# Performance work log

Measured on AMD Instinct MI355X. Metric: run time of the kernel, lower is better.

Reference implementation:

```python
import jax, jax.numpy as jnp
import numpy as np

B, T, D, V, SPK = 8, 4096, 512, 1024, 512
DECAY = 0.95
COARSE_SCALE = 0.2
RES_SCALE = 0.35
MAX_LS = 1.2
MAX_SIL = 0.35
COLD_RUNS = 2.0
MIN_DUR = 2.0


def gelu(x):
    return jax.nn.gelu(x, approximate=False)


def setup_inputs() -> dict:
    key = jax.random.key(0)
    ks = jax.random.split(key, 24)
    def n(k, shape, s=1.0):
        return jax.random.normal(k, shape, dtype=jnp.float32) * s
    inp = {}
    inp['content_units'] = jax.random.randint(ks[0], (B, T), 0, V)
    inp['log_anchor'] = n(ks[1], (B, T), 0.5) + 1.0
    inp['unit_mask'] = jax.random.randint(ks[2], (B, T), 0, 2)
    inp['sealed_mask'] = jax.random.randint(ks[3], (B, T), 0, 2)
    inp['silence_mask'] = jax.random.randint(ks[4], (B, T), 0, 2)
    inp['sep_hint'] = jax.random.uniform(ks[5], (B, T), dtype=jnp.float32)
    inp['edge_cue'] = jax.random.uniform(ks[6], (B, T), dtype=jnp.float32)
    inp['run_stability'] = jax.random.uniform(ks[7], (B, T), dtype=jnp.float32)
    inp['global_rate'] = n(ks[8], (B,), 0.1) + 1.0
    inp['local_rate_ema'] = n(ks[9], (B, 1), 0.1) + 1.0
    inp['spk_embed'] = n(ks[10], (B, SPK))
    s = 0.02
    inp['emb_table'] = n(ks[11], (V, D), s)
    inp['feat_W'] = n(ks[12], (5, D), s)      # scalar features -> dim
    inp['feat_b'] = jnp.zeros((D,), jnp.float32)
    inp['spk_W'] = n(ks[13], (SPK, D), s)
    inp['spk_b'] = jnp.zeros((D,), jnp.float32)
    inp['coarse_W1'] = n(ks[14], (D + 1, D), s)
    inp['coarse_b1'] = jnp.zeros((D,), jnp.float32)
    inp['coarse_W2'] = n(ks[15], (D, 1), s)
    inp['coarse_b2'] = jnp.zeros((1,), jnp.float32)
    inp['res_W1'] = n(ks[16], (2 * D + 1, D), s)
    inp['res_b1'] = jnp.zeros((D,), jnp.float32)
    inp['res_W2'] = n(ks[17], (D, 1), s)
    inp['res_b2'] = jnp.zeros((1,), jnp.float32)
    inp['src_rate_init'] = jnp.zeros((1,), jnp.float32)
    return inp


def _local_rate_scan(observed_log, speech_mask, init_rate):
    # Causal masked exponential-decay recurrence: emitted rate at t is the
    # state BEFORE observing step t (strictly causal); state only updates on
    # speech-commit steps.
    def step(rate, xs):
        obs, m = xs  # [B], [B]
        new = jnp.where(m > 0, DECAY * rate + (1.0 - DECAY) * obs, rate)
        return new, rate
    final, seq = jax.lax.scan(step, init_rate, (observed_log.T, speech_mask.T))
    return seq.T, final[:, None]  # [B,T], [B,1]


def reference(content_units, log_anchor, unit_mask, sealed_mask, silence_mask,
              sep_hint, edge_cue, run_stability, global_rate, local_rate_ema,
              spk_embed, emb_table, feat_W, feat_b, spk_W, spk_b,
              coarse_W1, coarse_b1, coarse_W2, coarse_b2,
              res_W1, res_b1, res_W2, res_b2, src_rate_init):
    f32 = jnp.float32
    mask = jnp.clip(unit_mask.astype(f32), 0.0, 1.0)
    sealed = jnp.clip(sealed_mask.astype(f32), 0.0, 1.0)
    silence = jnp.clip(silence_mask.astype(f32), 0.0, 1.0) * mask
    stability = jnp.clip(run_stability.astype(f32), 0.0, 1.0) * mask
    commit = mask * sealed
    sil_commit = commit * silence
    speech = commit * (1.0 - silence)

    la = log_anchor.astype(f32)
    rate_seq, rate_final = _local_rate_scan(la, speech, local_rate_ema[:, 0].astype(f32))

    # CausalUnitRunEncoder: token embedding + projection of per-step scalars
    feats = jnp.stack([la, rate_seq, silence, sep_hint.astype(f32), edge_cue.astype(f32)], axis=-1)  # [B,T,5]
    query = gelu(emb_table[content_units] + feats @ feat_W + feat_b) * mask[..., None]  # [B,T,D]

    grc = global_rate.astype(f32).reshape(-1, 1)[:, :1]  # [B,1]
    spk_ctx = jnp.tanh(spk_embed.astype(f32) @ spk_W + spk_b)  # [B,D]

    gsa = (grc - rate_seq) * commit  # global_shift_analytic [B,T]
    coarse_in = jnp.concatenate([spk_ctx, grc], axis=-1)  # [B,D+1]
    coarse_scalar = COARSE_SCALE * jnp.tanh((gelu(coarse_in @ coarse_W1 + coarse_b1) @ coarse_W2 + coarse_b2)[:, 0])  # [B]
    coarse_corr = coarse_scalar[:, None] * commit
    global_term = (gsa + coarse_corr) * commit

    # residual head: split first-layer weights to avoid materializing the concat
    Wq, Ws, wg = res_W1[:D], res_W1[D:2 * D], res_W1[2 * D]
    h = gelu(query @ Wq + (spk_ctx @ Ws)[:, None, :] + global_term[..., None] * wg + res_b1)  # [B,T,D]
    residual = RES_SCALE * jnp.tanh((h @ res_W2 + res_b2)[..., 0])  # [B,T]

    prefix_prev = jnp.maximum(jnp.cumsum(speech, axis=1) - speech, 0.0)
    cold_gate = jnp.clip(prefix_prev / COLD_RUNS, 0.0, 1.0)
    short_gate = jnp.clip((jnp.maximum(jnp.exp(la), 1.0) - 1.0) / max(1.0, MIN_DUR - 1.0), 0.0, 1.0)
    residual_gate = cold_gate * short_gate * stability * speech
    residual = residual * residual_gate

    pred_speech = jnp.clip(global_term + residual, -MAX_LS, MAX_LS) * speech
    pred_silence = jnp.clip(global_term, -MAX_SIL, MAX_SIL) * sil_commit
    pred = pred_speech + pred_silence  # unit_logstretch [B,T]
    return pred
```

## Files before the change

### kernel.cpp

```cpp
#include <hip/hip_runtime.h>
#include <hip/hip_bf16.h>

#define BB 8
#define TT 4096
#define DD 512
#define MM (BB*TT)
#define DECAYF 0.95f
#define OMDECAYF (1.0f - 0.95f)

typedef __attribute__((ext_vector_type(8))) short bf16x8;
typedef __attribute__((ext_vector_type(4))) float f32x4;

__device__ __forceinline__ float gelu_f(float x){
  return 0.5f * x * (1.0f + erff(x * 0.70710678118654752f));
}

__device__ __forceinline__ unsigned f2bf(float x){
  unsigned u = __float_as_uint(x);
  return (u + 0x7FFFu + ((u >> 16) & 1u)) >> 16;
}

__global__ __launch_bounds__(512) void pre_kernel(
    const float* __restrict__ spk_embed, const float* __restrict__ spk_W,
    const float* __restrict__ spk_b, const float* __restrict__ rW1,
    const float* __restrict__ la_g, const int* __restrict__ um,
    const int* __restrict__ sm, const int* __restrict__ zm,
    const float* __restrict__ stab_g, const float* __restrict__ lre,
    float* __restrict__ spk_ctx, unsigned short* __restrict__ wqt,
    float* __restrict__ rate_seq, float* __restrict__ rgate_a,
    int* __restrict__ active_list, int* __restrict__ acount)
{
  __shared__ float se[DD];
  __shared__ float red[8][64];
  __shared__ float tile[64][65];
  __shared__ float wAg[8], wBg[8], wSg[8];
  __shared__ int wcnt[8];
  int blk = blockIdx.x, t = threadIdx.x;
  int lane = t & 63, wid = t >> 6;

  if (blk < 64){
    int b = blk >> 3, d0 = (blk & 7) * 64;
    int dl = lane, ks = wid;
    se[t] = spk_embed[b*DD + t];
    __syncthreads();
    float a = 0.f;
    const float* wp = spk_W + (long)(ks*64)*DD + d0 + dl;
    #pragma unroll 8
    for (int k = 0; k < 64; ++k) a += se[ks*64 + k] * wp[(long)k*DD];
    red[ks][dl] = a;
    __syncthreads();
    if (t < 64){
      float s = spk_b[d0 + t];
      #pragma unroll
      for (int i = 0; i < 8; ++i) s += red[i][t];
      spk_ctx[b*DD + d0 + t] = tanhf(s);
    }
    return;
  }
  if (blk < 128){
    int tb = blk - 64;
    int nb = (tb & 7) * 64, kb = (tb >> 3) * 64;
    int tx = t & 63, ty = t >> 6;
    #pragma unroll
    for (int i = 0; i < 8; ++i){
      int k = ty + i*8;
      tile[k][tx] = rW1[(long)(kb + k)*DD + nb + tx];
    }
    __syncthreads();
    #pragma unroll
    for (int i = 0; i < 8; ++i){
      int nl = ty + i*8;
      wqt[(long)(nb + nl)*DD + kb + tx] = (unsigned short)f2bf(tile[tx][nl]);
    }
    return;
  }

  int b = blk - 128;
  int base = b*TT + t*8;
  float4 la0 = *(const float4*)(la_g + base);
  float4 la1 = *(const float4*)(la_g + base + 4);
  int4 u0 = *(const int4*)(um + base), u1 = *(const int4*)(um + base + 4);
  int4 s0 = *(const int4*)(sm + base), s1 = *(const int4*)(sm + base + 4);
  int4 z0 = *(const int4*)(zm + base), z1 = *(const int4*)(zm + base + 4);
  float4 st0 = *(const float4*)(stab_g + base), st1 = *(const float4*)(stab_g + base + 4);
  float lav[8] = {la0.x,la0.y,la0.z,la0.w,la1.x,la1.y,la1.z,la1.w};
  int uv[8] = {u0.x,u0.y,u0.z,u0.w,u1.x,u1.y,u1.z,u1.w};
  int sv[8] = {s0.x,s0.y,s0.z,s0.w,s1.x,s1.y,s1.z,s1.w};
  int zv[8] = {z0.x,z0.y,z0.z,z0.w,z1.x,z1.y,z1.z,z1.w};
  float stv_[8] = {st0.x,st0.y,st0.z,st0.w,st1.x,st1.y,st1.z,st1.w};
  float spv[8], stv[8];

  float A = 1.f, Bv = 0.f, S = 0.f;
  #pragma unroll
  for (int i = 0; i < 8; ++i){
    float m = uv[i] > 0 ? 1.f : 0.f;
    float sealed = sv[i] > 0 ? 1.f : 0.f;
    float sil = (zv[i] > 0 ? 1.f : 0.f) * m;
    float speech = (m * sealed) * (1.f - sil);
    spv[i] = speech;
    stv[i] = fminf(fmaxf(stv_[i], 0.f), 1.f) * m;
    if (speech > 0.f){
      Bv = DECAYF*Bv + OMDECAYF*lav[i];
      A *= DECAYF;
      S += 1.f;
    }
  }
  #pragma unroll
  for (int d = 1; d < 64; d <<= 1){
    float Au = __shfl_up(A, d, 64);
    float Bu = __shfl_up(Bv, d, 64);
    float Su = __shfl_up(S, d, 64);
    if (lane >= d){ Bv = A*Bu + Bv; A = A*Au; S += Su; }
  }
  if (lane == 63){ wAg[wid] = A; wBg[wid] = Bv; wSg[wid] = S; }
  float Ale = __shfl_up(A, 1, 64), Ble = __shfl_up(Bv, 1, 64), Sle = __shfl_up(S, 1, 64);
  if (lane == 0){ Ale = 1.f; Ble = 0.f; Sle = 0.f; }
  __syncthreads();
  float Awp = 1.f, Bwp = 0.f, Swp = 0.f;
  for (int w = 0; w < wid; ++w){
    Bwp = wAg[w]*Bwp + wBg[w];
    Awp = wAg[w]*Awp;
    Swp += wSg[w];
  }
  float Bex = Ale*Bwp + Ble;
  float Aex = Ale*Awp;
  float Sex = Swp + Sle;

  float rate = Aex*lre[b] + Bex;
  float ps = Sex;
  float ro[8], rg[8];
  #pragma unroll
  for (int i = 0; i < 8; ++i){
    ro[i] = rate;
    float cold = fminf(ps * 0.5f, 1.f);
    float shortg = fminf(fmaxf(expf(lav[i]) - 1.f, 0.f), 1.f);
    rg[i] = cold * shortg * stv[i] * spv[i];
    if (spv[i] > 0.f){
      rate = DECAYF*rate + OMDECAYF*lav[i];
      ps += 1.f;
    }
  }
  *(float4*)(rate_seq + base)     = make_float4(ro[0],ro[1],ro[2],ro[3]);
  *(float4*)(rate_seq + base + 4) = make_float4(ro[4],ro[5],ro[6],ro[7]);
  *(float4*)(rgate_a + base)      = make_float4(rg[0],rg[1],rg[2],rg[3]);
  *(float4*)(rgate_a + base + 4)  = make_float4(rg[4],rg[5],rg[6],rg[7]);

  int nact = 0;
  #pragma unroll
  for (int i = 0; i < 8; ++i) nact += (rg[i] != 0.f) ? 1 : 0;
  int inc = nact;
  #pragma unroll
  for (int d = 1; d < 64; d <<= 1){
    int u = __shfl_up(inc, d, 64);
    if (lane >= d) inc += u;
  }
  int myex = inc - nact;
  if (lane == 63) wcnt[wid] = inc;
  __syncthreads();
  int wbase = 0;
  for (int w = 0; w < wid; ++w) wbase += wcnt[w];
  int pos = wbase + myex;
  int* alist = active_list + b*TT;
  #pragma unroll
  for (int i = 0; i < 8; ++i){
    if (rg[i] != 0.f) alist[pos++] = base + i;
  }
  if (t == 0){
    int total = 0;
    #pragma unroll
    for (int w = 0; w < 8; ++w) total += wcnt[w];
    acount[b] = total;
  }
}

__global__ __launch_bounds__(512) void mid_kernel(
    const float* __restrict__ spk_ctx, const float* __restrict__ rW1,
    const float* __restrict__ cW1, const float* __restrict__ cb1,
    const float* __restrict__ cW2, const float* __restrict__ grate,
    const int* __restrict__ content, const float* __restrict__ la_g,
    const float* __restrict__ sep, const float* __restrict__ edge,
    const float* __restrict__ emb, const float* __restrict__ fW,
    const float* __restrict__ fb, const float* __restrict__ rate_seq,
    const int* __restrict__ active_list, const int* __restrict__ acount,
    float* __restrict__ s_vec, float* __restrict__ coarse_part,
    unsigned short* __restrict__ wsQ)
{
  int blk = blockIdx.x, t = threadIdx.x;
  int lane = t & 63, wid = t >> 6;

  if (blk < 64){
    __shared__ float sc[DD];
    __shared__ float red1[8][64];
    __shared__ float red2[8][64];
    int b = blk >> 3, d0 = (blk & 7) * 64;
    int dl = lane, ks = wid;
    sc[t] = spk_ctx[b*DD + t];
    __syncthreads();
    float a1 = 0.f, a2 = 0.f;
    const float* wsp = rW1 + (long)(DD + ks*64)*DD + d0 + dl;
    const float* wcp = cW1 + (long)(ks*64)*DD + d0 + dl;
    #pragma unroll 4
    for (int k = 0; k < 64; ++k){
      float s = sc[ks*64 + k];
      a1 += s * wsp[(long)k*DD];
      a2 += s * wcp[(long)k*DD];
    }
    red1[ks][dl] = a1; red2[ks][dl] = a2;
    __syncthreads();
    if (t < 64){
      int d = d0 + t;
      float s1 = 0.f;
      float s2 = cb1[d] + grate[b] * cW1[(long)DD*DD + d];
      #pragma unroll
      for (int i = 0; i < 8; ++i){ s1 += red1[i][t]; s2 += red2[i][t]; }
      s_vec[b*DD + d] = s1;
      float hv = gelu_f(s2) * cW2[d];
      #pragma unroll
      for (int sh = 1; sh < 64; sh <<= 1) hv += __shfl_xor(hv, sh, 64);
      if (t == 0) coarse_part[blk] = hv;
    }
    return;
  }

  int tb = blk - 64;
  int b = tb >> 6;
  int slot0 = (tb & 63) * 8 + wid;
  int cnt = acount[b];
  const int* alist = active_list + b*TT;
  int c0 = lane * 8;
  for (int j = slot0; j < cnt; j += 512){
    int gr = alist[j];
    float la = la_g[gr], rate = rate_seq[gr];
    float sepv = sep[gr], edgev = edge[gr];
    const float* er = emb + (long)content[gr]*DD + c0;
    float4 e0 = *(const float4*)(er), e1 = *(const float4*)(er + 4);
    float4 w00 = *(const float4*)(fW + c0),        w01 = *(const float4*)(fW + c0 + 4);
    float4 w10 = *(const float4*)(fW + DD + c0),   w11 = *(const float4*)(fW + DD + c0 + 4);
    float4 w30 = *(const float4*)(fW + 3*DD + c0), w31 = *(const float4*)(fW + 3*DD + c0 + 4);
    float4 w40 = *(const float4*)(fW + 4*DD + c0), w41 = *(const float4*)(fW + 4*DD + c0 + 4);
    float4 b0 = *(const float4*)(fb + c0), b1 = *(const float4*)(fb + c0 + 4);
    unsigned v0 = f2bf(gelu_f(e0.x + la*w00.x + rate*w10.x + sepv*w30.x + edgev*w40.x + b0.x));
    unsigned v1 = f2bf(gelu_f(e0.y + la*w00.y + rate*w10.y + sepv*w30.y + edgev*w40.y + b0.y));
    unsigned v2 = f2bf(gelu_f(e0.z + la*w00.z + rate*w10.z + sepv*w30.z + edgev*w40.z + b0.z));
    unsigned v3 = f2bf(gelu_f(e0.w + la*w00.w + rate*w10.w + sepv*w30.w + edgev*w40.w + b0.w));
    unsigned v4 = f2bf(gelu_f(e1.x + la*w01.x + rate*w11.x + sepv*w31.x + edgev*w41.x + b1.x));
    unsigned v5 = f2bf(gelu_f(e1.y + la*w01.y + rate*w11.y + sepv*w31.y + edgev*w41.y + b1.y));
    unsigned v6 = f2bf(gelu_f(e1.z + la*w01.z + rate*w11.z + sepv*w31.z + edgev*w41.z + b1.z));
    unsigned v7 = f2bf(gelu_f(e1.w + la*w01.w + rate*w11.w + sepv*w31.w + edgev*w41.w + b1.w));
    int4 pkv = make_int4((int)((v1 << 16) | v0), (int)((v3 << 16) | v2),
                         (int)((v5 << 16) | v4), (int)((v7 << 16) | v6));
    *(int4*)(wsQ + (long)(b*TT + j)*DD + c0) = pkv;
  }
}

__global__ __launch_bounds__(512) void main_kernel(
    const float* __restrict__ rate_seq, const unsigned short* __restrict__ wsQ,
    const unsigned short* __restrict__ wqt,
    const float* __restrict__ s_vec, const float* __restrict__ rW1,
    const float* __restrict__ rb1, const float* __restrict__ rW2,
    const float* __restrict__ rb2, const float* __restrict__ grate,
    const float* __restrict__ coarse_part, const float* __restrict__ cb2,
    const int* __restrict__ um, const int* __restrict__ sm,
    const int* __restrict__ zm,
    const float* __restrict__ rgate_a, const int* __restrict__ active_list,
    const int* __restrict__ acount, float* __restrict__ out)
{
  __shared__ unsigned short Af[16*32*32];
  __shared__ unsigned short Bs[2][512*32];
  __shared__ float part[8][32];
  __shared__ int seg_sh[3];
  int blk = blockIdx.x, tid = threadIdx.x, wid = tid >> 6, lane = tid & 63;

  if (tid < 128){
    int gr = blk*128 + tid;
    float rgv = rgate_a[gr];
    if (rgv == 0.f){
      int b = gr >> 12;
      float csum = cb2[0];
      #pragma unroll
      for (int c = 0; c < 8; ++c) csum += coarse_part[b*8 + c];
      float cs = 0.2f * tanhf(csum);
      float m = um[gr] > 0 ? 1.f : 0.f;
      float sealed = sm[gr] > 0 ? 1.f : 0.f;
      float sil = (zm[gr] > 0 ? 1.f : 0.f) * m;
      float commit = m * sealed;
      float speech = commit * (1.f - sil);
      float silc = commit * sil;
      float g = (grate[b] - rate_seq[gr] + cs) * commit;
      out[gr] = fminf(fmaxf(g, -1.2f), 1.2f) * speech
              + fminf(fmaxf(g, -0.35f), 0.35f) * silc;
    }
  }

  const char* wbase = (const char*)wqt;
  auto stageB = [&](unsigned short* dstbuf, int kc){
    int k0b = kc * 64;
    #pragma unroll
    for (int i = 0; i < 4; ++i){
      int j = wid*4 + i;
      int n = j*16 + (lane >> 2);
      int slot = (lane & 3) ^ ((n >> 1) & 3);
      const char* src = wbase + (long)n*1024 + k0b + slot*16;
      char* dst = (char*)dstbuf + j*1024 + (lane << 4);
      __builtin_amdgcn_global_load_lds(
          (const __attribute__((address_space(1))) void*)src,
          (__attribute__((address_space(3))) void*)dst, 16, 0, 0);
    }
  };

  for (int p = blk; ; p += 256){
    if (tid == 0){
      int cum = 0, sb = -1, slo = 0, scnt = 0;
      #pragma unroll
      for (int b = 0; b < BB; ++b){
        int c = acount[b];
        int nb = (c + 31) >> 5;
        if (sb < 0 && p < cum + nb){ sb = b; slo = (p - cum) * 32; scnt = c; }
        cum += nb;
      }
      seg_sh[0] = sb; seg_sh[1] = slo; seg_sh[2] = scnt;
    }
    __syncthreads();
    int seg_b = seg_sh[0], seg_lo = seg_sh[1], seg_cnt = seg_sh[2];
    if (seg_b < 0) break;
    const int* alist = active_list + seg_b*TT;
    const char* qseg = (const char*)(wsQ + (long)(seg_b*TT + seg_lo)*DD);

    float csum = cb2[0];
    #pragma unroll
    for (int c = 0; c < 8; ++c) csum += coarse_part[seg_b*8 + c];
    float cs = 0.2f * tanhf(csum);
    float grc = grate[seg_b];

    #pragma unroll
    for (int i = 0; i < 4; ++i){
      int idx = wid + i*8;
      int kcA = idx >> 1, half = idx & 1;
      int row = half*16 + (lane >> 2);
      int slot = (lane & 3) ^ ((row >> 1) & 3);
      const char* src = qseg + (long)row*1024 + kcA*64 + slot*16;
      char* dst = (char*)Af + kcA*2048 + half*1024 + (lane << 4);
      __builtin_amdgcn_global_load_lds(
          (const __attribute__((address_space(1))) void*)src,
          (__attribute__((address_space(3))) void*)dst, 16, 0, 0);
    }
    stageB(&Bs[0][0], 0);
    asm volatile("s_waitcnt vmcnt(0)" ::: "memory");
    __syncthreads();

    f32x4 acc[2][4];
    #pragma unroll
    for (int i = 0; i < 2; ++i)
      #pragma unroll
      for (int j = 0; j < 4; ++j) acc[i][j] = (f32x4){0.f,0.f,0.f,0.f};

    int rgp = lane >> 4, li = lane & 15;
    #pragma unroll
    for (int kc = 0; kc < 16; ++kc){
      if (kc < 15) stageB(&Bs[(kc+1)&1][0], kc+1);
      if (kc < 15) asm volatile("s_waitcnt vmcnt(4)" ::: "memory");
      else         asm volatile("s_waitcnt vmcnt(0)" ::: "memory");
      const char* bsb = (const char*)&Bs[kc&1][0];
      bf16x8 a[2], bb[4];
      #pragma unroll
      for (int mt = 0; mt < 2; ++mt){
        int row = mt*16 + li;
        int slot = rgp ^ ((row >> 1) & 3);
        a[mt] = *(const bf16x8*)((const char*)Af + kc*2048 + row*64 + (slot << 4));
      }
      #pragma unroll
      for (int nt = 0; nt < 4; ++nt){
        int n = wid*64 + nt*16 + li;
        int slot = rgp ^ ((n >> 1) & 3);
        bb[nt] = *(const bf16x8*)(bsb + n*64 + slot*16);
      }
      #pragma unroll
      for (int mt = 0; mt < 2; ++mt)
        #pragma unroll
        for (int nt = 0; nt < 4; ++nt)
          acc[mt][nt] = __builtin_amdgcn_mfma_f32_16x16x32_bf16(a[mt], bb[nt], acc[mt][nt], 0, 0, 0);
    }

    float svv[4], wgv[4], b1v[4], w2v[4];
    #pragma unroll
    for (int nt = 0; nt < 4; ++nt){
      int j = wid*64 + nt*16 + li;
      svv[nt] = s_vec[seg_b*DD + j];
      wgv[nt] = rW1[1024*DD + j];
      b1v[nt] = rb1[j];
      w2v[nt] = rW2[j];
    }
    #pragma unroll
    for (int mt = 0; mt < 2; ++mt){
      #pragma unroll
      for (int r = 0; r < 4; ++r){
        int row = mt*16 + rgp*4 + r;
        int q = seg_lo + row; if (q > seg_cnt-1) q = seg_cnt-1;
        int gr = alist[q];
        float gt = grc - rate_seq[gr] + cs;
        float s = 0.f;
        #pragma unroll
        for (int nt = 0; nt < 4; ++nt){
          float y = acc[mt][nt][r] + svv[nt] + gt*wgv[nt] + b1v[nt];
          s += gelu_f(y) * w2v[nt];
        }
        s += __shfl_xor(s, 1, 64);
        s += __shfl_xor(s, 2, 64);
        s += __shfl_xor(s, 4, 64);
        s += __shfl_xor(s, 8, 64);
        if (li == 0) part[wid][row] = s;
      }
    }
    __syncthreads();
    if (tid < 32){
      int q = seg_lo + tid;
      if (q < seg_cnt){
        int gr = alist[q];
        float s = 0.f;
        #pragma unroll
        for (int w = 0; w < 8; ++w) s += part[w][tid];
        float resid = 0.35f * tanhf(s + rb2[0]) * rgate_a[gr];
        float g = grc - rate_seq[gr] + cs;
        out[gr] = fminf(fmaxf(g + resid, -1.2f), 1.2f);
      }
    }
    __syncthreads();
  }
}

extern "C" void kernel_launch(void* const* d_in, const int* in_sizes, int n_in,
                              void* d_out, int out_size, void* d_ws, size_t ws_size,
                              hipStream_t stream)
{
  const int*   content = (const int*)  d_in[0];
  const float* la      = (const float*)d_in[1];
  const int*   um      = (const int*)  d_in[2];
  const int*   smk     = (const int*)  d_in[3];
  const int*   zm      = (const int*)  d_in[4];
  const float* sep     = (const float*)d_in[5];
  const float* edge    = (const float*)d_in[6];
  const float* stab    = (const float*)d_in[7];
  const float* grate   = (const float*)d_in[8];
  const float* lre     = (const float*)d_in[9];
  const float* spk_e   = (const float*)d_in[10];
  const float* emb     = (const float*)d_in[11];
  const float* fW      = (const float*)d_in[12];
  const float* fb      = (const float*)d_in[13];
  const float* spk_W   = (const float*)d_in[14];
  const float* spk_b   = (const float*)d_in[15];
  const float* cW1     = (const float*)d_in[16];
  const float* cb1     = (const float*)d_in[17];
  const float* cW2     = (const float*)d_in[18];
  const float* cb2     = (const float*)d_in[19];
  const float* rW1     = (const float*)d_in[20];
  const float* rb1     = (const float*)d_in[21];
  const float* rW2     = (const float*)d_in[22];
  const float* rb2     = (const float*)d_in[23];

  char* w = (char*)d_ws;
  unsigned short* wsQ   = (unsigned short*)(w);
  unsigned short* wsWqT = (unsigned short*)(w + 33554432);
  size_t off = 33554432 + 524288;
  float* rate_seq = (float*)(w + off); off += MM*4;
  float* rgate_a  = (float*)(w + off); off += MM*4;
  int*   active_list = (int*)(w + off); off += MM*4;
  float* s_vec    = (float*)(w + off); off += BB*DD*4;
  float* spk_ctx  = (float*)(w + off); off += BB*DD*4;
  float* coarse_part = (float*)(w + off); off += 64*4;
  int*   acount   = (int*)(w + off); off += 256;

  pre_kernel<<<136, 512, 0, stream>>>(spk_e, spk_W, spk_b, rW1,
      la, um, smk, zm, stab, lre,
      spk_ctx, wsWqT, rate_seq, rgate_a, active_list, acount);
  mid_kernel<<<576, 512, 0, stream>>>(spk_ctx, rW1, cW1, cb1, cW2, grate,
      content, la, sep, edge, emb, fW, fb, rate_seq, active_list, acount,
      s_vec, coarse_part, wsQ);
  main_kernel<<<256, 512, 0, stream>>>(rate_seq, wsQ, wsWqT,
      s_vec, rW1, rb1, rW2, rb2, grate, coarse_part, cb2,
      um, smk, zm, rgate_a, active_list, acount, (float*)d_out);
}
```

Measured before the change: 35.32 us.

## Pack per-token gating data into float4 and precompute segment map for main kernel

The pre kernel now writes one packed float4 per token: the global term without the coarse correction, the speech mask, the silence mask and the residual gate. The main kernel reads this instead of re-reading the three mask arrays, rate_seq, grate and rgate_a. An extra block in the mid kernel precomputes a segment-to-batch map, so the main kernel no longer needs a per-iteration thread-0 scan and barrier. The tail clamp on segment rows is dropped. A memset of the active list is added so padded rows read index 0, which is safe because token 0 always has a zero gate. The cost is an extra memset launch and a larger packed buffer in the workspace.

```diff
diff --git a/kernel.cpp b/kernel.cpp
--- a/kernel.cpp
+++ b/kernel.cpp
@@ -26,8 +26,9 @@
     const float* __restrict__ la_g, const int* __restrict__ um,
     const int* __restrict__ sm, const int* __restrict__ zm,
     const float* __restrict__ stab_g, const float* __restrict__ lre,
+    const float* __restrict__ grate,
     float* __restrict__ spk_ctx, unsigned short* __restrict__ wqt,
-    float* __restrict__ rate_seq, float* __restrict__ rgate_a,
+    float* __restrict__ rate_seq, float4* __restrict__ pk4,
     int* __restrict__ active_list, int* __restrict__ acount)
 {
   __shared__ float se[DD];
@@ -88,7 +89,7 @@
   int sv[8] = {s0.x,s0.y,s0.z,s0.w,s1.x,s1.y,s1.z,s1.w};
   int zv[8] = {z0.x,z0.y,z0.z,z0.w,z1.x,z1.y,z1.z,z1.w};
   float stv_[8] = {st0.x,st0.y,st0.z,st0.w,st1.x,st1.y,st1.z,st1.w};
-  float spv[8], stv[8];
+  float spv[8], slv[8], stv[8];
 
   float A = 1.f, Bv = 0.f, S = 0.f;
   #pragma unroll
@@ -96,8 +97,9 @@
     float m = uv[i] > 0 ? 1.f : 0.f;
     float sealed = sv[i] > 0 ? 1.f : 0.f;
     float sil = (zv[i] > 0 ? 1.f : 0.f) * m;
-    float speech = (m * sealed) * (1.f - sil);
-    spv[i] = speech;
+    float commit = m * sealed;
+    float speech = commit * (1.f - sil);
+    spv[i] = speech; slv[i] = commit * sil;
     stv[i] = fminf(fmaxf(stv_[i], 0.f), 1.f) * m;
     if (speech > 0.f){
       Bv = DECAYF*Bv + OMDECAYF*lav[i];
@@ -128,13 +130,17 @@
 
   float rate = Aex*lre[b] + Bex;
   float ps = Sex;
+  float grc = grate[b];
   float ro[8], rg[8];
   #pragma unroll
   for (int i = 0; i < 8; ++i){
     ro[i] = rate;
+    float commit = spv[i] + slv[i];
+    float gA = (grc - rate) * commit;
     float cold = fminf(ps * 0.5f, 1.f);
     float shortg = fminf(fmaxf(expf(lav[i]) - 1.f, 0.f), 1.f);
     rg[i] = cold * shortg * stv[i] * spv[i];
+    pk4[base + i] = make_float4(gA, spv[i], slv[i], rg[i]);
     if (spv[i] > 0.f){
       rate = DECAYF*rate + OMDECAYF*lav[i];
       ps += 1.f;
@@ -142,8 +148,6 @@
   }
   *(float4*)(rate_seq + base)     = make_float4(ro[0],ro[1],ro[2],ro[3]);
   *(float4*)(rate_seq + base + 4) = make_float4(ro[4],ro[5],ro[6],ro[7]);
-  *(float4*)(rgate_a + base)      = make_float4(rg[0],rg[1],rg[2],rg[3]);
-  *(float4*)(rgate_a + base + 4)  = make_float4(rg[4],rg[5],rg[6],rg[7]);
 
   int nact = 0;
   #pragma unroll
@@ -183,7 +187,7 @@
     const float* __restrict__ fb, const float* __restrict__ rate_seq,
     const int* __restrict__ active_list, const int* __restrict__ acount,
     float* __restrict__ s_vec, float* __restrict__ coarse_part,
-    unsigned short* __restrict__ wsQ)
+    unsigned short* __restrict__ wsQ, int2* __restrict__ segmap)
 {
   int blk = blockIdx.x, t = threadIdx.x;
   int lane = t & 63, wid = t >> 6;
@@ -218,6 +222,25 @@
       #pragma unroll
       for (int sh = 1; sh < 64; sh <<= 1) hv += __shfl_xor(hv, sh, 64);
       if (t == 0) coarse_part[blk] = hv;
+    }
+    return;
+  }
+  if (blk == 576){
+    int cnts[BB], offs[BB];
+    int cum = 0;
+    #pragma unroll
+    for (int b = 0; b < BB; ++b){
+      cnts[b] = (acount[b] + 31) >> 5;
+      offs[b] = cum;
+      cum += cnts[b];
+    }
+    for (int i = t; i < 1024; i += 512){
+      int2 e = make_int2(-1, 0);
+      #pragma unroll
+      for (int b = 0; b < BB; ++b){
+        if (i >= offs[b] && i < offs[b] + cnts[b]) e = make_int2(b, (i - offs[b]) * 32);
+      }
+      segmap[i] = e;
     }
     return;
   }
@@ -254,41 +277,32 @@
 }
 
 __global__ __launch_bounds__(512) void main_kernel(
-    const float* __restrict__ rate_seq, const unsigned short* __restrict__ wsQ,
-    const unsigned short* __restrict__ wqt,
+    const unsigned short* __restrict__ wsQ, const unsigned short* __restrict__ wqt,
     const float* __restrict__ s_vec, const float* __restrict__ rW1,
     const float* __restrict__ rb1, const float* __restrict__ rW2,
-    const float* __restrict__ rb2, const float* __restrict__ grate,
+    const float* __restrict__ rb2,
     const float* __restrict__ coarse_part, const float* __restrict__ cb2,
-    const int* __restrict__ um, const int* __restrict__ sm,
-    const int* __restrict__ zm,
-    const float* __restrict__ rgate_a, const int* __restrict__ active_list,
-    const int* __restrict__ acount, float* __restrict__ out)
+    const float4* __restrict__ pk4, const int* __restrict__ active_list,
+    const int2* __restrict__ segmap, float* __restrict__ out)
 {
   __shared__ unsigned short Af[16*32*32];
   __shared__ unsigned short Bs[2][512*32];
   __shared__ float part[8][32];
-  __shared__ int seg_sh[3];
   int blk = blockIdx.x, tid = threadIdx.x, wid = tid >> 6, lane = tid & 63;
 
   if (tid < 128){
     int gr = blk*128 + tid;
-    float rgv = rgate_a[gr];
-    if (rgv == 0.f){
+    float4 pk = pk4[gr];
+    if (pk.w == 0.f){
       int b = gr >> 12;
       float csum = cb2[0];
       #pragma unroll
       for (int c = 0; c < 8; ++c) csum += coarse_part[b*8 + c];
       float cs = 0.2f * tanhf(csum);
-      float m = um[gr] > 0 ? 1.f : 0.f;
-      float sealed = sm[gr] > 0 ? 1.f : 0.f;
-      float sil = (zm[gr] > 0 ? 1.f : 0.f) * m;
-      float commit = m * sealed;
-      float speech = commit * (1.f - sil);
-      float silc = commit * sil;
-      float g = (grate[b] - rate_seq[gr] + cs) * commit;
-      out[gr] = fminf(fmaxf(g, -1.2f), 1.2f) * speech
-              + fminf(fmaxf(g, -0.35f), 0.35f) * silc;
+      float commit = pk.y + pk.z;
+      float g = pk.x + cs * commit;
+      out[gr] = fminf(fmaxf(g, -1.2f), 1.2f) * pk.y
+              + fminf(fmaxf(g, -0.35f), 0.35f) * pk.z;
     }
   }
 
@@ -308,21 +322,10 @@
     }
   };
 
-  for (int p = blk; ; p += 256){
-    if (tid == 0){
-      int cum = 0, sb = -1, slo = 0, scnt = 0;
-      #pragma unroll
-      for (int b = 0; b < BB; ++b){
-        int c = acount[b];
-        int nb = (c + 31) >> 5;
-        if (sb < 0 && p < cum + nb){ sb = b; slo = (p - cum) * 32; scnt = c; }
-        cum += nb;
-      }
-      seg_sh[0] = sb; seg_sh[1] = slo; seg_sh[2] = scnt;
-    }
-    __syncthreads();
-    int seg_b = seg_sh[0], seg_lo = seg_sh[1], seg_cnt = seg_sh[2];
-    if (seg_b < 0) break;
+  for (int p = blk; p < 1024; p += 256){
+    int2 seg = segmap[p];
+    if (seg.x < 0) break;
+    int seg_b = seg.x, seg_lo = seg.y;
     const int* alist = active_list + seg_b*TT;
     const char* qseg = (const char*)(wsQ + (long)(seg_b*TT + seg_lo)*DD);
 
@@ -330,7 +333,6 @@
     #pragma unroll
     for (int c = 0; c < 8; ++c) csum += coarse_part[seg_b*8 + c];
     float cs = 0.2f * tanhf(csum);
-    float grc = grate[seg_b];
 
     #pragma unroll
     for (int i = 0; i < 4; ++i){
@@ -395,9 +397,9 @@
       #pragma unroll
       for (int r = 0; r < 4; ++r){
         int row = mt*16 + rgp*4 + r;
-        int q = seg_lo + row; if (q > seg_cnt-1) q = seg_cnt-1;
+        int q = seg_lo + row;
         int gr = alist[q];
-        float gt = grc - rate_seq[gr] + cs;
+        float gt = pk4[gr].x + cs;
         float s = 0.f;
         #pragma unroll
         for (int nt = 0; nt < 4; ++nt){
@@ -414,13 +416,14 @@
     __syncthreads();
     if (tid < 32){
       int q = seg_lo + tid;
-      if (q < seg_cnt){
-        int gr = alist[q];
+      int gr = alist[q];
+      float4 pk = pk4[gr];
+      if (pk.w != 0.f){
         float s = 0.f;
         #pragma unroll
         for (int w = 0; w < 8; ++w) s += part[w][tid];
-        float resid = 0.35f * tanhf(s + rb2[0]) * rgate_a[gr];
-        float g = grc - rate_seq[gr] + cs;
+        float resid = 0.35f * tanhf(s + rb2[0]) * pk.w;
+        float g = pk.x + cs;
         out[gr] = fminf(fmaxf(g + resid, -1.2f), 1.2f);
       }
     }
@@ -462,20 +465,22 @@
   unsigned short* wsWqT = (unsigned short*)(w + 33554432);
   size_t off = 33554432 + 524288;
   float* rate_seq = (float*)(w + off); off += MM*4;
-  float* rgate_a  = (float*)(w + off); off += MM*4;
+  float4* pk4     = (float4*)(w + off); off += MM*16;
   int*   active_list = (int*)(w + off); off += MM*4;
   float* s_vec    = (float*)(w + off); off += BB*DD*4;
   float* spk_ctx  = (float*)(w + off); off += BB*DD*4;
   float* coarse_part = (float*)(w + off); off += 64*4;
   int*   acount   = (int*)(w + off); off += 256;
-
+  int2*  segmap   = (int2*)(w + off); off += 1024*8;
+
+  hipMemsetAsync(active_list, 0, MM*4, stream);
   pre_kernel<<<136, 512, 0, stream>>>(spk_e, spk_W, spk_b, rW1,
-      la, um, smk, zm, stab, lre,
-      spk_ctx, wsWqT, rate_seq, rgate_a, active_list, acount);
-  mid_kernel<<<576, 512, 0, stream>>>(spk_ctx, rW1, cW1, cb1, cW2, grate,
+      la, um, smk, zm, stab, lre, grate,
+      spk_ctx, wsWqT, rate_seq, pk4, active_list, acount);
+  mid_kernel<<<577, 512, 0, stream>>>(spk_ctx, rW1, cW1, cb1, cW2, grate,
       content, la, sep, edge, emb, fW, fb, rate_seq, active_list, acount,
-      s_vec, coarse_part, wsQ);
-  main_kernel<<<256, 512, 0, stream>>>(rate_seq, wsQ, wsWqT,
-      s_vec, rW1, rb1, rW2, rb2, grate, coarse_part, cb2,
-      um, smk, zm, rgate_a, active_list, acount, (float*)d_out);
-}
+      s_vec, coarse_part, wsQ, segmap);
+  main_kernel<<<256, 512, 0, stream>>>(wsQ, wsWqT,
+      s_vec, rW1, rb1, rW2, rb2, coarse_part, cb2,
+      pk4, active_list, segmap, (float*)d_out);
+}
```

New measurement: 41.51 us. 1.18x slower.
